# Kernel optimization log

Hardware: AMD Instinct MI355X
Metric: run time of the kernel (lower is better)

## Reference

```python
import jax, jax.numpy as jnp
import numpy as np

HEAD_DIM = 256
N_HEADS = 8
ROPE_BASE = 10000.0
EPS = 1e-6


def _rms(x):
    xf = x.astype(jnp.float32)
    return xf * jax.lax.rsqrt(jnp.mean(xf * xf, axis=-1, keepdims=True) + EPS)


def _rotate_half(x):
    x1, x2 = jnp.split(x, 2, axis=-1)
    return jnp.concatenate([-x2, x1], axis=-1)


def _mlp(h, wg, wu, wd):
    # Gemma gated MLP with gelu_pytorch_tanh activation
    return (jax.nn.gelu(h @ wg, approximate=True) * (h @ wu)) @ wd


def _qkv(h, wq, wk, wv):
    B, S, _ = h.shape
    q = (h @ wq).reshape(B, S, N_HEADS, HEAD_DIM).transpose(0, 2, 1, 3)  # [B,H,S,Dh]
    k = (h @ wk).reshape(B, S, HEAD_DIM)                                  # MQA: 1 kv head
    v = (h @ wv).reshape(B, S, HEAD_DIM)
    return q, k, v


def _forward(x_prefix, x_expert, attention_mask, adarms_cond, position_ids,
             p_ln1, p_wq, p_wk, p_wv, p_wo, p_ln2, p_wgate, p_wup, p_wdown,
             e_ada1_w, e_ada1_b, e_wq, e_wk, e_wv, e_wo, e_ada2_w, e_ada2_b,
             e_wgate, e_wup, e_wdown):
    B, S1, Dp = x_prefix.shape
    S2 = x_expert.shape[1]

    # --- pre-attention norms: plain Gemma RMSNorm (prefix), AdaRMS (expert) ---
    h_p = _rms(x_prefix) * (1.0 + p_ln1)
    mod1 = adarms_cond @ e_ada1_w + e_ada1_b                  # [B, 3*De]
    sc1, sh1, g1 = jnp.split(mod1, 3, axis=-1)
    h_e = _rms(x_expert) * (1.0 + sc1[:, None]) + sh1[:, None]
    gate1_e = g1[:, None]                                      # [B,1,De]

    # --- concatenated QKV across the two streams ---
    q_p, k_p, v_p = _qkv(h_p, p_wq, p_wk, p_wv)
    q_e, k_e, v_e = _qkv(h_e, e_wq, e_wk, e_wv)
    q = jnp.concatenate([q_p, q_e], axis=2)                    # [B,H,S,Dh]
    k = jnp.concatenate([k_p, k_e], axis=1)                    # [B,S,Dh]
    v = jnp.concatenate([v_p, v_e], axis=1)

    # --- rotary embedding on joint positions ---
    inv_freq = 1.0 / (ROPE_BASE ** (jnp.arange(0, HEAD_DIM, 2, dtype=jnp.float32) / HEAD_DIM))
    ang = position_ids.astype(jnp.float32)[..., None] * inv_freq
    emb = jnp.concatenate([ang, ang], axis=-1)                 # [B,S,Dh]
    cos, sin = jnp.cos(emb), jnp.sin(emb)
    q = q * cos[:, None] + _rotate_half(q) * sin[:, None]
    k = k * cos + _rotate_half(k) * sin

    # --- eager MQA attention ---
    scaling = HEAD_DIM ** -0.5
    scores = jnp.einsum('bhqd,bkd->bhqk', q, k) * scaling + attention_mask
    probs = jax.nn.softmax(scores.astype(jnp.float32), axis=-1)
    att = jnp.einsum('bhqk,bkd->bhqd', probs, v)
    att = att.transpose(0, 2, 1, 3).reshape(B, S1 + S2, N_HEADS * HEAD_DIM)

    # --- prefix stream: o_proj, residual, RMSNorm, gated MLP, residual ---
    res_p = x_prefix + att[:, :S1] @ p_wo
    h2_p = _rms(res_p) * (1.0 + p_ln2)
    out_p = res_p + _mlp(h2_p, p_wgate, p_wup, p_wdown)

    # --- expert stream: gated residuals from AdaRMS ---
    res_e = x_expert + gate1_e * (att[:, S1:] @ e_wo)
    mod2 = adarms_cond @ e_ada2_w + e_ada2_b
    sc2, sh2, g2 = jnp.split(mod2, 3, axis=-1)
    h2_e = _rms(res_e) * (1.0 + sc2[:, None]) + sh2[:, None]
    out_e = res_e + g2[:, None] * _mlp(h2_e, e_wgate, e_wup, e_wdown)
    return out_p, out_e


def setup_inputs() -> dict:
    key = jax.random.key(0)
    ks = iter(jax.random.split(key, 32))
    B, S1, S2 = 4, 768, 64
    Dp, De, Dh, H = 2048, 1024, 256, 8
    Fp, Fe = 16384, 4096

    def w(shape, s=0.02):
        return jax.random.normal(next(ks), shape, dtype=jnp.float32) * s

    return dict(
        x_prefix=jax.random.normal(next(ks), (B, S1, Dp), dtype=jnp.float32),
        x_expert=jax.random.normal(next(ks), (B, S2, De), dtype=jnp.float32),
        attention_mask=jnp.zeros((B, 1, S1 + S2, S1 + S2), dtype=jnp.float32),
        adarms_cond=jax.random.normal(next(ks), (B, De), dtype=jnp.float32),
        position_ids=jnp.sort(jax.random.randint(next(ks), (B, S1 + S2), 0, S1 + S2), axis=-1),
        p_ln1=jnp.zeros((Dp,), jnp.float32),
        p_wq=w((Dp, H * Dh)), p_wk=w((Dp, Dh)), p_wv=w((Dp, Dh)), p_wo=w((H * Dh, Dp)),
        p_ln2=jnp.zeros((Dp,), jnp.float32),
        p_wgate=w((Dp, Fp)), p_wup=w((Dp, Fp)), p_wdown=w((Fp, Dp)),
        e_ada1_w=w((De, 3 * De)), e_ada1_b=jnp.zeros((3 * De,), jnp.float32),
        e_wq=w((De, H * Dh)), e_wk=w((De, Dh)), e_wv=w((De, Dh)), e_wo=w((H * Dh, De)),
        e_ada2_w=w((De, 3 * De)), e_ada2_b=jnp.zeros((3 * De,), jnp.float32),
        e_wgate=w((De, Fe)), e_wup=w((De, Fe)), e_wdown=w((Fe, De)),
    )


def reference(x_prefix, x_expert, attention_mask, adarms_cond, position_ids,
              p_ln1, p_wq, p_wk, p_wv, p_wo, p_ln2, p_wgate, p_wup, p_wdown,
              e_ada1_w, e_ada1_b, e_wq, e_wk, e_wv, e_wo, e_ada2_w, e_ada2_b,
              e_wgate, e_wup, e_wdown):
    return _forward(x_prefix, x_expert, attention_mask, adarms_cond, position_ids,
                    p_ln1, p_wq, p_wk, p_wv, p_wo, p_ln2, p_wgate, p_wup, p_wdown,
                    e_ada1_w, e_ada1_b, e_wq, e_wk, e_wv, e_wo, e_ada2_w, e_ada2_b,
                    e_wgate, e_wup, e_wdown)
```

## Files before the change

kernel.cpp:

```cpp
#include <hip/hip_runtime.h>
#include <stdint.h>

typedef unsigned short ushort_t;
typedef __attribute__((ext_vector_type(8))) short short8;
typedef __attribute__((ext_vector_type(4))) float f32x4;

#define DEVINL __device__ __forceinline__

DEVINL ushort_t f2bf(float f){
  union { float f; uint32_t u; } v; v.f = f;
  uint32_t u = v.u;
  uint32_t r = (u + 0x7fffu + ((u >> 16) & 1u)) >> 16;
  return (ushort_t)r;
}
DEVINL float bf2f(ushort_t h){
  union { uint32_t u; float f; } v; v.u = ((uint32_t)h) << 16;
  return v.f;
}
DEVINL f32x4 mfma16(short8 a, short8 b, f32x4 c){
  return __builtin_amdgcn_mfma_f32_16x16x32_bf16(a, b, c, 0, 0, 0);
}
DEVINL void gload_lds16(const void* g, void* l){
  __builtin_amdgcn_global_load_lds((const __attribute__((address_space(1))) void*)g,
                                   (__attribute__((address_space(3))) void*)l, 16, 0, 0);
}
DEVINL float gelu_tanh(float x){
  return 0.5f * x * (1.f + tanhf(0.7978845608028654f * (x + 0.044715f * x * x * x)));
}

#define BAR() __builtin_amdgcn_s_barrier()
#define LGK0() asm volatile("s_waitcnt lgkmcnt(0)" ::: "memory")
#define VMC4() asm volatile("s_waitcnt vmcnt(4)" ::: "memory")
#define VMC0() asm volatile("s_waitcnt vmcnt(0)" ::: "memory")
#define PRIO1() __builtin_amdgcn_s_setprio(1)
#define PRIO0() __builtin_amdgcn_s_setprio(0)

__global__ void transpose_bf16(const float* __restrict__ W, ushort_t* __restrict__ Wt,
                               int K, int N)
{
  __shared__ ushort_t tile[64 * 65];
  const int t = threadIdx.x;
  const int k0 = blockIdx.y * 64, n0 = blockIdx.x * 64;
#pragma unroll
  for (int rr = 0; rr < 4; ++rr){
    const int row = rr * 16 + (t >> 4);
    const int c4 = (t & 15) * 4;
    float4 v = *(const float4*)&W[(size_t)(k0 + row) * N + n0 + c4];
    ushort_t* dst = &tile[row * 65 + c4];
    dst[0] = f2bf(v.x); dst[1] = f2bf(v.y); dst[2] = f2bf(v.z); dst[3] = f2bf(v.w);
  }
  __syncthreads();
  const int n = t >> 2, kc = (t & 3) * 16;
  __align__(16) ushort_t tmp[16];
#pragma unroll
  for (int j = 0; j < 16; ++j) tmp[j] = tile[(kc + j) * 65 + n];
  ushort_t* out = &Wt[(size_t)(n0 + n) * K + k0 + kc];
  *(short8*)&out[0] = *(short8*)&tmp[0];
  *(short8*)&out[8] = *(short8*)&tmp[8];
}

__global__ void mod_kernel(const float* __restrict__ cond,
                           const float* __restrict__ w1, const float* __restrict__ b1,
                           const float* __restrict__ w2, const float* __restrict__ b2,
                           float* __restrict__ mod1, float* __restrict__ mod2)
{
  __shared__ float cs[1024];
  const int bid = blockIdx.x, tid = threadIdx.x;
  const int which = bid / 48, rem = bid % 48, b = rem / 12, j0 = (rem % 12) * 256;
  const float* W = which ? w2 : w1;
  const float* bias = which ? b2 : b1;
  float* out = which ? mod2 : mod1;
#pragma unroll
  for (int i = 0; i < 4; ++i) cs[i * 256 + tid] = cond[b * 1024 + i * 256 + tid];
  __syncthreads();
  const int j = j0 + tid;
  float acc = bias[j];
  for (int k = 0; k < 1024; ++k) acc = fmaf(cs[k], W[(size_t)k * 3072 + j], acc);
  out[b * 3072 + j] = acc;
}

__global__ void rms_kernel(const float* __restrict__ x, ushort_t* __restrict__ out, int D,
                           const float* __restrict__ sw, const float* __restrict__ sh,
                           int mod_rpb, int mod_stride)
{
  const int row = blockIdx.x, tid = threadIdx.x;
  const float* xr = x + (size_t)row * D;
  const int nc = D >> 10;
  float ss = 0.f;
  for (int c = 0; c < nc; ++c){
    float4 v = *(const float4*)&xr[c * 1024 + tid * 4];
    ss += v.x * v.x + v.y * v.y + v.z * v.z + v.w * v.w;
  }
  for (int o = 32; o > 0; o >>= 1) ss += __shfl_xor(ss, o);
  __shared__ float red[4];
  if ((tid & 63) == 0) red[tid >> 6] = ss;
  __syncthreads();
  const float scale = rsqrtf((red[0] + red[1] + red[2] + red[3]) / (float)D + 1e-6f);
  const float* swp = sw;
  const float* shp = sh;
  if (mod_rpb){
    int bb = row / mod_rpb;
    swp += (size_t)bb * mod_stride;
    if (shp) shp += (size_t)bb * mod_stride;
  }
  for (int c = 0; c < nc; ++c){
    const int d = c * 1024 + tid * 4;
    float4 v = *(const float4*)&xr[d];
    float vv[4] = {v.x, v.y, v.z, v.w};
#pragma unroll
    for (int i = 0; i < 4; ++i){
      float tv = vv[i] * scale * (1.f + swp[d + i]);
      if (shp) tv += shp[d + i];
      out[(size_t)row * D + d + i] = f2bf(tv);
    }
  }
}

__global__ void rope_kernel(const ushort_t* __restrict__ qkv_p, const ushort_t* __restrict__ qkv_e,
                            const int* __restrict__ pos_ids,
                            ushort_t* __restrict__ q_all, ushort_t* __restrict__ k_all,
                            ushort_t* __restrict__ vT)
{
  const int tok = blockIdx.x, tid = threadIdx.x;
  int b, s;
  const ushort_t* src;
  if (tok < 3072){ b = tok / 768; s = tok - b * 768; src = qkv_p + (size_t)tok * 2560; }
  else { int te = tok - 3072; b = te >> 6; s = 768 + (te & 63); src = qkv_e + (size_t)te * 2560; }
  const int pos = pos_ids[b * 832 + s];
  __shared__ float cs[128], sn[128];
  if (tid < 128){
    float f = powf(10000.f, -(float)tid * (1.f / 128.f));
    float a = (float)pos * f;
    cs[tid] = cosf(a); sn[tid] = sinf(a);
  }
  __syncthreads();
#pragma unroll
  for (int c = 0; c < 10; ++c){
    const int n = c * 256 + tid;
    const float v = bf2f(src[n]);
    if (n < 2048){
      const int h = n >> 8, d = n & 255;
      const float o = bf2f(src[(h << 8) + ((d < 128) ? (d + 128) : (d - 128))]);
      const int dd = d & 127;
      const float r = (d < 128) ? v * cs[dd] - o * sn[dd] : v * cs[dd] + o * sn[dd];
      q_all[(((size_t)(b * 8 + h)) * 832 + s) * 256 + d] = f2bf(r);
    } else if (n < 2304){
      const int d = n - 2048;
      const float o = bf2f(src[2048 + ((d < 128) ? (d + 128) : (d - 128))]);
      const int dd = d & 127;
      const float r = (d < 128) ? v * cs[dd] - o * sn[dd] : v * cs[dd] + o * sn[dd];
      k_all[((size_t)(b * 832) + s) * 256 + d] = f2bf(r);
    } else {
      const int d = n - 2304;
      vT[((size_t)(b * 256) + d) * 832 + s] = src[n];
    }
  }
}

__global__ void __launch_bounds__(256, 2)
attn_kernel(const ushort_t* __restrict__ q_all, const ushort_t* __restrict__ k_all,
            const ushort_t* __restrict__ vT, const float* __restrict__ mask,
            ushort_t* __restrict__ att)
{
  __shared__ __align__(16) ushort_t Ks[64 * 256];
  __shared__ __align__(16) ushort_t Vs[256 * 64];
  __shared__ __align__(16) ushort_t Ps[4][16 * 72];
  const int tid = threadIdx.x, lane = tid & 63, wid = tid >> 6;
  const int l15 = lane & 15, lg = lane >> 4;
  const int qt = blockIdx.x, h = blockIdx.y, b = blockIdx.z;
  const int q0 = qt * 64 + wid * 16;

  short8 qf[8];
  {
    const ushort_t* qr = q_all + (((size_t)(b * 8 + h) * 832) + q0 + l15) * 256;
#pragma unroll
    for (int s = 0; s < 8; ++s) qf[s] = *(const short8*)&qr[s * 32 + lg * 8];
  }

  f32x4 accO[16] = {};
  float mrow[4] = {-3.0e38f, -3.0e38f, -3.0e38f, -3.0e38f};
  float lrow[4] = {0.f, 0.f, 0.f, 0.f};

  for (int kt = 0; kt < 13; ++kt){
    const int s0 = kt * 64;
#pragma unroll
    for (int i = 0; i < 8; ++i){
      const int o = i * 256 + tid;
      gload_lds16(k_all + ((size_t)(b * 832) + s0 + (o >> 5)) * 256 + (o & 31) * 8, &Ks[o * 8]);
      gload_lds16(vT + ((size_t)(b * 256) + (o >> 3)) * 832 + s0 + (o & 7) * 8, &Vs[o * 8]);
    }
    __syncthreads();

    f32x4 sc[4] = {};
#pragma unroll
    for (int s = 0; s < 8; ++s){
#pragma unroll
      for (int nf = 0; nf < 4; ++nf){
        short8 kb = *(const short8*)&Ks[(nf * 16 + l15) * 256 + s * 32 + lg * 8];
        sc[nf] = mfma16(qf[s], kb, sc[nf]);
      }
    }
#pragma unroll
    for (int nf = 0; nf < 4; ++nf){
#pragma unroll
      for (int r = 0; r < 4; ++r){
        const int q = q0 + lg * 4 + r;
        const int kk = s0 + nf * 16 + l15;
        sc[nf][r] = sc[nf][r] * 0.0625f + mask[((size_t)b * 832 + q) * 832 + kk];
      }
    }
    float al[4];
#pragma unroll
    for (int r = 0; r < 4; ++r){
      float tm = fmaxf(fmaxf(sc[0][r], sc[1][r]), fmaxf(sc[2][r], sc[3][r]));
      tm = fmaxf(tm, __shfl_xor(tm, 1));
      tm = fmaxf(tm, __shfl_xor(tm, 2));
      tm = fmaxf(tm, __shfl_xor(tm, 4));
      tm = fmaxf(tm, __shfl_xor(tm, 8));
      const float mnew = fmaxf(mrow[r], tm);
      al[r] = __expf(mrow[r] - mnew);
      mrow[r] = mnew;
      float rs = 0.f;
#pragma unroll
      for (int nf = 0; nf < 4; ++nf){
        const float p = __expf(sc[nf][r] - mnew);
        rs += p;
        Ps[wid][(lg * 4 + r) * 72 + nf * 16 + l15] = f2bf(p);
      }
      rs += __shfl_xor(rs, 1);
      rs += __shfl_xor(rs, 2);
      rs += __shfl_xor(rs, 4);
      rs += __shfl_xor(rs, 8);
      lrow[r] = lrow[r] * al[r] + rs;
    }
#pragma unroll
    for (int nd = 0; nd < 16; ++nd){
#pragma unroll
      for (int r = 0; r < 4; ++r) accO[nd][r] *= al[r];
    }
#pragma unroll
    for (int ks = 0; ks < 2; ++ks){
      short8 pa = *(const short8*)&Ps[wid][l15 * 72 + ks * 32 + lg * 8];
#pragma unroll
      for (int nd = 0; nd < 16; ++nd){
        short8 vb = *(const short8*)&Vs[(nd * 16 + l15) * 64 + ks * 32 + lg * 8];
        accO[nd] = mfma16(pa, vb, accO[nd]);
      }
    }
    __syncthreads();
  }
#pragma unroll
  for (int nd = 0; nd < 16; ++nd){
#pragma unroll
    for (int r = 0; r < 4; ++r){
      const int q = q0 + lg * 4 + r;
      const int d = nd * 16 + l15;
      att[((size_t)(b * 832) + q) * 2048 + h * 256 + d] = f2bf(accO[nd][r] / lrow[r]);
    }
  }
}

template<int EPI>
__global__ void __launch_bounds__(256, 2)
gemm_bt(const ushort_t* __restrict__ A, int lda, int a_rpb, int a_bstride, int a_r0,
        const ushort_t* __restrict__ Bt, int ldb,
        void* __restrict__ Cv, int N, int K,
        const void* __restrict__ Xv,
        const float* __restrict__ gatep, int gate_stride, int gate_rpb,
        size_t pstride)
{
  __shared__ __align__(16) ushort_t As[128 * 64];
  __shared__ __align__(16) ushort_t Bs[128 * 64];
  const int tid = threadIdx.x;
  const int lane = tid & 63;
  const int l15 = lane & 15, lg = lane >> 4;
  const int wid = tid >> 6;
  const int wm = (wid >> 1) * 64, wn = (wid & 1) * 64;
  const int m0 = blockIdx.y * 128, n0 = blockIdx.x * 128;
  const int z = blockIdx.z;
  const int kbeg = z * K, kend = z * K + K;

  size_t abase[4], bbase[4];
  const int k8 = (tid & 7) * 8;
#pragma unroll
  for (int i = 0; i < 4; ++i){
    const int row = (i * 256 + tid) >> 3;
    const int r = m0 + row;
    const int bb = r / a_rpb;
    const int arow = bb * a_bstride + a_r0 + (r - bb * a_rpb);
    abase[i] = (size_t)arow * lda + k8;
    bbase[i] = (size_t)(n0 + row) * ldb + k8;
  }

  f32x4 acc[4][4] = {};

  for (int kt = kbeg; kt < kend; kt += 64){
#pragma unroll
    for (int i = 0; i < 4; ++i){
      gload_lds16(A + abase[i] + kt, &As[(i * 256 + tid) * 8]);
      gload_lds16(Bt + bbase[i] + kt, &Bs[(i * 256 + tid) * 8]);
    }
    __syncthreads();
#pragma unroll
    for (int s = 0; s < 2; ++s){
      const int ko = s * 32 + lg * 8;
      short8 af[4], bfr[4];
#pragma unroll
      for (int i = 0; i < 4; ++i) af[i] = *(const short8*)&As[(wm + i * 16 + l15) * 64 + ko];
#pragma unroll
      for (int j = 0; j < 4; ++j) bfr[j] = *(const short8*)&Bs[(wn + j * 16 + l15) * 64 + ko];
#pragma unroll
      for (int i = 0; i < 4; ++i)
#pragma unroll
        for (int j = 0; j < 4; ++j)
          acc[i][j] = mfma16(af[i], bfr[j], acc[i][j]);
    }
    __syncthreads();
  }

#pragma unroll
  for (int i = 0; i < 4; ++i){
#pragma unroll
    for (int r = 0; r < 4; ++r){
      const int m = m0 + wm + i * 16 + lg * 4 + r;
#pragma unroll
      for (int j = 0; j < 4; ++j){
        const int n = n0 + wn + j * 16 + l15;
        const size_t idx = (size_t)m * N + n;
        const float v = acc[i][j][r];
        if (EPI == 0){
          ((ushort_t*)Cv)[idx] = f2bf(v);
        } else if (EPI == 1){
          const float g = bf2f(((const ushort_t*)Xv)[idx]);
          ((ushort_t*)Cv)[idx] = f2bf(gelu_tanh(g) * v);
        } else if (EPI == 2){
          ((float*)Cv)[idx] = ((const float*)Xv)[idx] + v;
        } else if (EPI == 3){
          const int bb = m / gate_rpb;
          ((float*)Cv)[idx] = ((const float*)Xv)[idx] + gatep[(size_t)bb * gate_stride + n] * v;
        } else {
          ((float*)Cv)[(size_t)z * pstride + idx] = v;
        }
      }
    }
  }
}

#define MMAQ(AF, BF, MQ, NQ) \
  { _Pragma("unroll") for (int i_ = 0; i_ < 4; ++i_){ \
      _Pragma("unroll") for (int j_ = 0; j_ < 2; ++j_){ \
        _Pragma("unroll") for (int s_ = 0; s_ < 2; ++s_){ \
          acc[(MQ)*4 + i_][(NQ)*2 + j_] = \
            mfma16(AF[i_][s_], BF[j_][s_], acc[(MQ)*4 + i_][(NQ)*2 + j_]); } } } }

#define READA(F, BUF, OA) \
  { _Pragma("unroll") for (int i_ = 0; i_ < 4; ++i_){ \
      _Pragma("unroll") for (int s_ = 0; s_ < 2; ++s_){ \
        F[i_][s_] = *(const short8*)&(BUF)[OA[i_][s_]]; } } }

#define READB(F, BUF, OB) \
  { _Pragma("unroll") for (int j_ = 0; j_ < 2; ++j_){ \
      _Pragma("unroll") for (int s_ = 0; s_ < 2; ++s_){ \
        F[j_][s_] = *(const short8*)&(BUF)[OB[j_][s_]]; } } }

template<int EPI>
__global__ void __launch_bounds__(512, 1)
gemm8(const ushort_t* __restrict__ A, int lda,
      const ushort_t* __restrict__ Bt, int ldb,
      void* __restrict__ Cv, int N, int klen,
      const void* __restrict__ Xv, size_t pstride)
{
  __shared__ __align__(16) ushort_t As[2][256 * 64];
  __shared__ __align__(16) ushort_t Bs[2][256 * 64];

  const int tid = threadIdx.x;
  const int lane = tid & 63, wid = tid >> 6;
  const int l15 = lane & 15, lg = lane >> 4;
  const int wm = (wid >> 2) * 128, wn = (wid & 3) * 64;

  const int gx = gridDim.x, gy = gridDim.y, nwg = gx * gy;
  const int orig = blockIdx.y * gx + blockIdx.x;
  const int q = nwg >> 3, r = nwg & 7;
  const int xcd = orig & 7, lo = orig >> 3;
  const int wg = (xcd < r ? xcd * (q + 1) : r * (q + 1) + (xcd - r) * q) + lo;
  const int m0 = (wg % gy) * 256, n0 = (wg / gy) * 256;
  const int z = blockIdx.z;
  const size_t k0 = (size_t)z * klen;
  const int NT = klen >> 6;

  uint32_t offA0[4][2], offA1[4][2], offB0[2][2], offB1[2][2];
#pragma unroll
  for (int i = 0; i < 4; ++i){
#pragma unroll
    for (int s = 0; s < 2; ++s){
      int r0 = wm + 0 * 64 + i * 16 + l15;
      int r1 = wm + 1 * 64 + i * 16 + l15;
      offA0[i][s] = r0 * 64 + (((s * 4 + lg) ^ (r0 & 7)) << 3);
      offA1[i][s] = r1 * 64 + (((s * 4 + lg) ^ (r1 & 7)) << 3);
    }
  }
#pragma unroll
  for (int j = 0; j < 2; ++j){
#pragma unroll
    for (int s = 0; s < 2; ++s){
      int r0 = wn + 0 * 32 + j * 16 + l15;
      int r1 = wn + 1 * 32 + j * 16 + l15;
      offB0[j][s] = r0 * 64 + (((s * 4 + lg) ^ (r0 & 7)) << 3);
      offB1[j][s] = r1 * 64 + (((s * 4 + lg) ^ (r1 & 7)) << 3);
    }
  }

  const ushort_t* gptr[4][2];
  uint32_t ldso[2];
#pragma unroll
  for (int c = 0; c < 2; ++c){
    const int idx = c * 512 + tid;
    const int row = idx >> 3, slot = idx & 7;
    const uint32_t sw = (uint32_t)((slot ^ (row & 7)) << 3);
    ldso[c] = (uint32_t)idx * 8;
    gptr[0][c] = A  + (size_t)(m0 + row) * lda + k0 + sw;
    gptr[1][c] = A  + (size_t)(m0 + 128 + row) * lda + k0 + sw;
    gptr[2][c] = Bt + (size_t)(n0 + row) * ldb + k0 + sw;
    gptr[3][c] = Bt + (size_t)(n0 + 128 + row) * ldb + k0 + sw;
  }

  auto stage = [&](int buf, int half, int kt){
    ushort_t* base = (half < 2) ? &As[buf][(half & 1) * 8192] : &Bs[buf][(half & 1) * 8192];
#pragma unroll
    for (int c = 0; c < 2; ++c)
      gload_lds16(gptr[half][c] + kt, base + ldso[c]);
  };

  stage(0, 0, 0); stage(0, 1, 0); stage(0, 2, 0); stage(0, 3, 0);
  if (NT > 1){ stage(1, 2, 64); stage(1, 3, 64); VMC4(); } else { VMC0(); }
  BAR();

  short8 af[4][2], bq0[2][2], bq1[2][2];
  f32x4 acc[8][4] = {};

  for (int t = 0; t < NT; ++t){
    const int cur = t & 1, nxt = cur ^ 1;
    const int kc1 = (t + 1) << 6, kc2 = (t + 2) << 6;
    const ushort_t* Ac = As[cur];
    const ushort_t* Bc = Bs[cur];
    READA(af, Ac, offA0);
    READB(bq0, Bc, offB0);
    READB(bq1, Bc, offB1);
    if (t + 1 < NT){ stage(nxt, 0, kc1); stage(nxt, 1, kc1); }
    BAR(); LGK0();
    PRIO1(); MMAQ(af, bq0, 0, 0); MMAQ(af, bq1, 0, 1); PRIO0(); BAR();
    READA(af, Ac, offA1);
    if (t + 2 < NT){ stage(cur, 2, kc2); stage(cur, 3, kc2); VMC4(); } else { VMC0(); }
    BAR(); LGK0();
    PRIO1(); MMAQ(af, bq1, 1, 1); MMAQ(af, bq0, 1, 0); PRIO0(); BAR();
  }

#pragma unroll
  for (int i = 0; i < 8; ++i){
#pragma unroll
    for (int rr = 0; rr < 4; ++rr){
      const int m = m0 + wm + i * 16 + lg * 4 + rr;
#pragma unroll
      for (int j = 0; j < 4; ++j){
        const int n = n0 + wn + j * 16 + l15;
        const size_t idx = (size_t)m * N + n;
        const float v = acc[i][j][rr];
        if (EPI == 0){
          ((ushort_t*)Cv)[idx] = f2bf(v);
        } else if (EPI == 1){
          const float g = bf2f(((const ushort_t*)Xv)[idx]);
          ((ushort_t*)Cv)[idx] = f2bf(gelu_tanh(g) * v);
        } else {
          ((float*)Cv)[(size_t)z * pstride + idx] = v;
        }
      }
    }
  }
}

__global__ void reduce4(const float* __restrict__ part, const float* __restrict__ res,
                        float* __restrict__ out, int total4, size_t pstride)
{
  int i = blockIdx.x * blockDim.x + threadIdx.x;
  const int stride = gridDim.x * blockDim.x;
  for (; i < total4; i += stride){
    const size_t e = (size_t)i * 4;
    float4 a = *(const float4*)&res[e];
#pragma unroll
    for (int z = 0; z < 4; ++z){
      float4 p = *(const float4*)&part[(size_t)z * pstride + e];
      a.x += p.x; a.y += p.y; a.z += p.z; a.w += p.w;
    }
    *(float4*)&out[e] = a;
  }
}

__global__ void fuse_gelu(const float* __restrict__ pg, const float* __restrict__ pu,
                          ushort_t* __restrict__ out, int total4, size_t pstride)
{
  int i = blockIdx.x * blockDim.x + threadIdx.x;
  const int stride = gridDim.x * blockDim.x;
  for (; i < total4; i += stride){
    const size_t e = (size_t)i * 4;
    float4 g = *(const float4*)&pg[e];
    float4 u = *(const float4*)&pu[e];
#pragma unroll
    for (int z = 1; z < 4; ++z){
      float4 a = *(const float4*)&pg[(size_t)z * pstride + e];
      float4 b = *(const float4*)&pu[(size_t)z * pstride + e];
      g.x += a.x; g.y += a.y; g.z += a.z; g.w += a.w;
      u.x += b.x; u.y += b.y; u.z += b.z; u.w += b.w;
    }
    out[e + 0] = f2bf(gelu_tanh(g.x) * u.x);
    out[e + 1] = f2bf(gelu_tanh(g.y) * u.y);
    out[e + 2] = f2bf(gelu_tanh(g.z) * u.z);
    out[e + 3] = f2bf(gelu_tanh(g.w) * u.w);
  }
}

__global__ void reduce_gated(const float* __restrict__ part, size_t pstride, int nz,
                             const float* __restrict__ base, const float* __restrict__ gate,
                             int gstride, int rpb, int N,
                             float* __restrict__ out, int total4)
{
  int i = blockIdx.x * blockDim.x + threadIdx.x;
  const int stride = gridDim.x * blockDim.x;
  for (; i < total4; i += stride){
    const size_t e = (size_t)i * 4;
    const int row = (int)(e / N), n = (int)(e % N);
    const int b = row / rpb;
    float4 s = *(const float4*)&part[e];
    for (int z = 1; z < nz; ++z){
      float4 p = *(const float4*)&part[(size_t)z * pstride + e];
      s.x += p.x; s.y += p.y; s.z += p.z; s.w += p.w;
    }
    float4 bs = *(const float4*)&base[e];
    const float* gp = &gate[(size_t)b * gstride + n];
    bs.x += gp[0] * s.x; bs.y += gp[1] * s.y; bs.z += gp[2] * s.z; bs.w += gp[3] * s.w;
    *(float4*)&out[e] = bs;
  }
}

extern "C" void kernel_launch(void* const* d_in, const int* in_sizes, int n_in,
                              void* d_out, int out_size, void* d_ws, size_t ws_size,
                              hipStream_t stream)
{
  const float* x_prefix = (const float*)d_in[0];
  const float* x_expert = (const float*)d_in[1];
  const float* mask     = (const float*)d_in[2];
  const float* cond     = (const float*)d_in[3];
  const int*   pos      = (const int*)d_in[4];
  const float* p_ln1    = (const float*)d_in[5];
  const float* p_wq     = (const float*)d_in[6];
  const float* p_wk     = (const float*)d_in[7];
  const float* p_wv     = (const float*)d_in[8];
  const float* p_wo     = (const float*)d_in[9];
  const float* p_ln2    = (const float*)d_in[10];
  const float* p_wgate  = (const float*)d_in[11];
  const float* p_wup    = (const float*)d_in[12];
  const float* p_wdown  = (const float*)d_in[13];
  const float* e_ada1_w = (const float*)d_in[14];
  const float* e_ada1_b = (const float*)d_in[15];
  const float* e_wq     = (const float*)d_in[16];
  const float* e_wk     = (const float*)d_in[17];
  const float* e_wv     = (const float*)d_in[18];
  const float* e_wo     = (const float*)d_in[19];
  const float* e_ada2_w = (const float*)d_in[20];
  const float* e_ada2_b = (const float*)d_in[21];
  const float* e_wgate  = (const float*)d_in[22];
  const float* e_wup    = (const float*)d_in[23];
  const float* e_wdown  = (const float*)d_in[24];

  char* ws = (char*)d_ws;
  size_t off = 0;
  auto alloc = [&](size_t bytes) -> char* {
    char* p = ws + off;
    off += bytes;
    off = (off + 255) & ~(size_t)255;
    return p;
  };

  ushort_t* t_wqkv_p  = (ushort_t*)alloc((size_t)2560 * 2048 * 2);
  ushort_t* t_wo_p    = (ushort_t*)alloc((size_t)2048 * 2048 * 2);
  ushort_t* t_wgate_p = (ushort_t*)alloc((size_t)16384 * 2048 * 2);
  ushort_t* t_wup_p   = (ushort_t*)alloc((size_t)16384 * 2048 * 2);
  ushort_t* t_wdown_p = (ushort_t*)alloc((size_t)2048 * 16384 * 2);
  ushort_t* t_wqkv_e  = (ushort_t*)alloc((size_t)2560 * 1024 * 2);
  ushort_t* t_wo_e    = (ushort_t*)alloc((size_t)1024 * 2048 * 2);
  ushort_t* t_wgate_e = (ushort_t*)alloc((size_t)4096 * 1024 * 2);
  ushort_t* t_wup_e   = (ushort_t*)alloc((size_t)4096 * 1024 * 2);
  ushort_t* t_wdown_e = (ushort_t*)alloc((size_t)1024 * 4096 * 2);
  float* mod1 = (float*)alloc((size_t)4 * 3072 * 4);
  float* mod2 = (float*)alloc((size_t)4 * 3072 * 4);
  float* res_p = (float*)alloc((size_t)3072 * 2048 * 4);
  float* res_e = (float*)alloc((size_t)256 * 1024 * 4);
  ushort_t* h2_p = (ushort_t*)alloc((size_t)3072 * 2048 * 2);
  ushort_t* h2_e = (ushort_t*)alloc((size_t)256 * 1024 * 2);
  ushort_t* g_e  = (ushort_t*)alloc((size_t)256 * 4096 * 2);

  const size_t zone_off = off;
  ushort_t* h_p   = (ushort_t*)alloc((size_t)3072 * 2048 * 2);
  ushort_t* h_e   = (ushort_t*)alloc((size_t)256 * 1024 * 2);
  ushort_t* qkv_p = (ushort_t*)alloc((size_t)3072 * 2560 * 2);
  ushort_t* qkv_e = (ushort_t*)alloc((size_t)256 * 2560 * 2);
  ushort_t* q_all = (ushort_t*)alloc((size_t)4 * 8 * 832 * 256 * 2);
  ushort_t* k_all = (ushort_t*)alloc((size_t)4 * 832 * 256 * 2);
  ushort_t* vTb   = (ushort_t*)alloc((size_t)4 * 256 * 832 * 2);
  ushort_t* att   = (ushort_t*)alloc((size_t)4 * 832 * 2048 * 2);
  const size_t phase1_end = off;
  ushort_t* g_p = (ushort_t*)(ws + zone_off);

  float* partials = (float*)t_wgate_p;
  const size_t PSTRIDE_P = (size_t)3072 * 2048;
  float* pwo = (float*)(ws + zone_off);
  const size_t PSTRIDE_E = (size_t)256 * 1024;
  float* pg = (float*)t_wgate_p;
  float* pu = pg + (size_t)4 * 256 * 4096;
  float* pd = pu + (size_t)4 * 256 * 4096;
  const size_t PSTRIDE_GE = (size_t)256 * 4096;

  const size_t g_p_end = zone_off + (size_t)3072 * 16384 * 2;
  const size_t needed = (phase1_end > g_p_end) ? phase1_end : g_p_end;
  if (ws_size < needed) return;

  const int BIG = 1 << 30;

  transpose_bf16<<<dim3(2048/64, 2048/64), 256, 0, stream>>>(p_wq, t_wqkv_p, 2048, 2048);
  transpose_bf16<<<dim3(256/64, 2048/64), 256, 0, stream>>>(p_wk, t_wqkv_p + (size_t)2048*2048, 2048, 256);
  transpose_bf16<<<dim3(256/64, 2048/64), 256, 0, stream>>>(p_wv, t_wqkv_p + (size_t)2304*2048, 2048, 256);
  transpose_bf16<<<dim3(2048/64, 2048/64), 256, 0, stream>>>(p_wo, t_wo_p, 2048, 2048);
  transpose_bf16<<<dim3(16384/64, 2048/64), 256, 0, stream>>>(p_wgate, t_wgate_p, 2048, 16384);
  transpose_bf16<<<dim3(16384/64, 2048/64), 256, 0, stream>>>(p_wup, t_wup_p, 2048, 16384);
  transpose_bf16<<<dim3(2048/64, 16384/64), 256, 0, stream>>>(p_wdown, t_wdown_p, 16384, 2048);
  transpose_bf16<<<dim3(2048/64, 1024/64), 256, 0, stream>>>(e_wq, t_wqkv_e, 1024, 2048);
  transpose_bf16<<<dim3(256/64, 1024/64), 256, 0, stream>>>(e_wk, t_wqkv_e + (size_t)2048*1024, 1024, 256);
  transpose_bf16<<<dim3(256/64, 1024/64), 256, 0, stream>>>(e_wv, t_wqkv_e + (size_t)2304*1024, 1024, 256);
  transpose_bf16<<<dim3(1024/64, 2048/64), 256, 0, stream>>>(e_wo, t_wo_e, 2048, 1024);
  transpose_bf16<<<dim3(4096/64, 1024/64), 256, 0, stream>>>(e_wgate, t_wgate_e, 1024, 4096);
  transpose_bf16<<<dim3(4096/64, 1024/64), 256, 0, stream>>>(e_wup, t_wup_e, 1024, 4096);
  transpose_bf16<<<dim3(1024/64, 4096/64), 256, 0, stream>>>(e_wdown, t_wdown_e, 4096, 1024);

  mod_kernel<<<96, 256, 0, stream>>>(cond, e_ada1_w, e_ada1_b, e_ada2_w, e_ada2_b, mod1, mod2);

  rms_kernel<<<3072, 256, 0, stream>>>(x_prefix, h_p, 2048, p_ln1, nullptr, 0, 0);
  rms_kernel<<<256, 256, 0, stream>>>(x_expert, h_e, 1024, mod1, mod1 + 1024, 64, 3072);

  gemm_bt<0><<<dim3(20, 24), 256, 0, stream>>>(h_p, 2048, BIG, 0, 0, t_wqkv_p, 2048,
                                               qkv_p, 2560, 2048, nullptr, nullptr, 0, 1, 0);
  gemm_bt<0><<<dim3(20, 2), 256, 0, stream>>>(h_e, 1024, BIG, 0, 0, t_wqkv_e, 1024,
                                              qkv_e, 2560, 1024, nullptr, nullptr, 0, 1, 0);

  rope_kernel<<<3328, 256, 0, stream>>>(qkv_p, qkv_e, pos, q_all, k_all, vTb);

  attn_kernel<<<dim3(13, 8, 4), 256, 0, stream>>>(q_all, k_all, vTb, mask, att);

  gemm_bt<2><<<dim3(16, 24), 256, 0, stream>>>(att, 2048, 768, 832, 0, t_wo_p, 2048,
                                               res_p, 2048, 2048, x_prefix, nullptr, 0, 1, 0);
  gemm_bt<4><<<dim3(8, 2, 4), 256, 0, stream>>>(att, 2048, 64, 832, 768, t_wo_e, 2048,
                                                pwo, 1024, 512, nullptr, nullptr, 0, 1, PSTRIDE_E);
  reduce_gated<<<256, 256, 0, stream>>>(pwo, PSTRIDE_E, 4, x_expert, mod1 + 2048, 3072, 64, 1024,
                                        res_e, (256 * 1024) / 4);

  rms_kernel<<<3072, 256, 0, stream>>>(res_p, h2_p, 2048, p_ln2, nullptr, 0, 0);
  rms_kernel<<<256, 256, 0, stream>>>(res_e, h2_e, 1024, mod2, mod2 + 1024, 64, 3072);

  gemm8<0><<<dim3(64, 12, 1), 512, 0, stream>>>(h2_p, 2048, t_wgate_p, 2048,
                                                g_p, 16384, 2048, nullptr, 0);
  gemm8<1><<<dim3(64, 12, 1), 512, 0, stream>>>(h2_p, 2048, t_wup_p, 2048,
                                                g_p, 16384, 2048, g_p, 0);
  gemm8<4><<<dim3(8, 12, 4), 512, 0, stream>>>(g_p, 16384, t_wdown_p, 16384,
                                               partials, 2048, 4096, nullptr, PSTRIDE_P);
  reduce4<<<2048, 256, 0, stream>>>(partials, res_p, (float*)d_out,
                                    (3072 * 2048) / 4, PSTRIDE_P);

  gemm_bt<4><<<dim3(32, 2, 4), 256, 0, stream>>>(h2_e, 1024, BIG, 0, 0, t_wgate_e, 1024,
                                                 pg, 4096, 256, nullptr, nullptr, 0, 1, PSTRIDE_GE);
  gemm_bt<4><<<dim3(32, 2, 4), 256, 0, stream>>>(h2_e, 1024, BIG, 0, 0, t_wup_e, 1024,
                                                 pu, 4096, 256, nullptr, nullptr, 0, 1, PSTRIDE_GE);
  fuse_gelu<<<1024, 256, 0, stream>>>(pg, pu, g_e, (256 * 4096) / 4, PSTRIDE_GE);
  gemm_bt<4><<<dim3(8, 2, 8), 256, 0, stream>>>(g_e, 4096, BIG, 0, 0, t_wdown_e, 4096,
                                                pd, 1024, 512, nullptr, nullptr, 0, 1, PSTRIDE_E);
  reduce_gated<<<256, 256, 0, stream>>>(pd, PSTRIDE_E, 8, res_e, mod2 + 2048, 3072, 64, 1024,
                                        (float*)d_out + (size_t)3072 * 2048, (256 * 1024) / 4);
}
```

Before: 1.293 ms.

## Restructure GEMM main loop into eight-phase ping-pong with finer-grained staged loads

The double-buffered GEMM mainloop is unrolled by two and split into eight MFMA quadrant phases. Each phase issues one quarter-tile global-to-LDS load, in the style of the HipKittens 8-wave schedule, with a vmcnt(6) wait so more loads stay in flight. The goal is to overlap memory traffic with MFMA work more evenly and shorten the stalls between compute blocks. It adds more barriers and assumes NT is even and at least 2, since the prologue now stages the second buffer unconditionally.

```diff
diff --git a/kernel.cpp b/kernel.cpp
--- a/kernel.cpp
+++ b/kernel.cpp
@@ -30,6 +30,7 @@
 
 #define BAR() __builtin_amdgcn_s_barrier()
 #define LGK0() asm volatile("s_waitcnt lgkmcnt(0)" ::: "memory")
+#define VMC6() asm volatile("s_waitcnt vmcnt(6)" ::: "memory")
 #define VMC4() asm volatile("s_waitcnt vmcnt(4)" ::: "memory")
 #define VMC0() asm volatile("s_waitcnt vmcnt(0)" ::: "memory")
 #define PRIO1() __builtin_amdgcn_s_setprio(1)
@@ -431,28 +432,48 @@
       gload_lds16(gptr[half][c] + kt, base + ldso[c]);
   };
 
-  stage(0, 0, 0); stage(0, 1, 0); stage(0, 2, 0); stage(0, 3, 0);
-  if (NT > 1){ stage(1, 2, 64); stage(1, 3, 64); VMC4(); } else { VMC0(); }
-  BAR();
+  stage(0, 2, 0); stage(0, 3, 0); stage(0, 0, 0); stage(0, 1, 0);
+  stage(1, 2, 64); stage(1, 3, 64); stage(1, 0, 64);
+  VMC6(); BAR();
 
   short8 af[4][2], bq0[2][2], bq1[2][2];
   f32x4 acc[8][4] = {};
 
-  for (int t = 0; t < NT; ++t){
-    const int cur = t & 1, nxt = cur ^ 1;
-    const int kc1 = (t + 1) << 6, kc2 = (t + 2) << 6;
-    const ushort_t* Ac = As[cur];
-    const ushort_t* Bc = Bs[cur];
-    READA(af, Ac, offA0);
-    READB(bq0, Bc, offB0);
-    READB(bq1, Bc, offB1);
-    if (t + 1 < NT){ stage(nxt, 0, kc1); stage(nxt, 1, kc1); }
+  for (int t = 0; t < NT; t += 2){
+    const int kc1 = (t + 1) << 6, kc2 = (t + 2) << 6, kc3 = (t + 3) << 6;
+    const bool more = (t + 2 < NT);
+    READA(af, As[0], offA0);
+    READB(bq0, Bs[0], offB0);
+    stage(1, 1, kc1);
     BAR(); LGK0();
-    PRIO1(); MMAQ(af, bq0, 0, 0); MMAQ(af, bq1, 0, 1); PRIO0(); BAR();
-    READA(af, Ac, offA1);
-    if (t + 2 < NT){ stage(cur, 2, kc2); stage(cur, 3, kc2); VMC4(); } else { VMC0(); }
+    PRIO1(); MMAQ(af, bq0, 0, 0); PRIO0(); BAR();
+    READB(bq1, Bs[0], offB1);
+    if (more) stage(0, 2, kc2);
     BAR(); LGK0();
-    PRIO1(); MMAQ(af, bq1, 1, 1); MMAQ(af, bq0, 1, 0); PRIO0(); BAR();
+    PRIO1(); MMAQ(af, bq1, 0, 1); PRIO0(); BAR();
+    READA(af, As[0], offA1);
+    if (more) stage(0, 3, kc2);
+    BAR(); LGK0();
+    PRIO1(); MMAQ(af, bq1, 1, 1); PRIO0(); BAR();
+    if (more){ stage(0, 0, kc2); VMC6(); } else { VMC0(); }
+    BAR();
+    PRIO1(); MMAQ(af, bq0, 1, 0); PRIO0(); BAR();
+    READA(af, As[1], offA0);
+    READB(bq0, Bs[1], offB0);
+    if (more) stage(0, 1, kc2);
+    BAR(); LGK0();
+    PRIO1(); MMAQ(af, bq0, 0, 0); PRIO0(); BAR();
+    READB(bq1, Bs[1], offB1);
+    if (more) stage(1, 2, kc3);
+    BAR(); LGK0();
+    PRIO1(); MMAQ(af, bq1, 0, 1); PRIO0(); BAR();
+    READA(af, As[1], offA1);
+    if (more) stage(1, 3, kc3);
+    BAR(); LGK0();
+    PRIO1(); MMAQ(af, bq1, 1, 1); PRIO0(); BAR();
+    if (more){ stage(1, 0, kc3); VMC6(); } else { VMC0(); }
+    BAR();
+    PRIO1(); MMAQ(af, bq0, 1, 0); PRIO0(); BAR();
   }
 
 #pragma unroll
```

Result: slower. 1.350 ms (+4.3%).

## Fuse prefix gate and up projections into one dual-accumulator GEMM kernel

Applied to the files above, without the earlier changes.

Replaces the two separate gate and up GEMMs for the prefix MLP, which wrote the gate output to memory and reread it for the GELU product, with one kernel that loads the shared activation tile once and accumulates both projections, applying GELU-tanh times up in the epilogue. This saves a full bf16 intermediate write and read and one reload of the activations. The new kernel is simple: single-buffered LDS with no overlap of loads and compute, 128x128 tiles, and doubled accumulator registers. Compared with the tuned 512-thread gemm8 it may lose pipelining efficiency and occupancy.

```diff
diff --git a/kernel.cpp b/kernel.cpp
--- a/kernel.cpp
+++ b/kernel.cpp
@@ -341,6 +341,77 @@
         } else {
           ((float*)Cv)[(size_t)z * pstride + idx] = v;
         }
+      }
+    }
+  }
+}
+
+__global__ void __launch_bounds__(256)
+gemm_gu(const ushort_t* __restrict__ A, int lda,
+        const ushort_t* __restrict__ Bg, const ushort_t* __restrict__ Bu, int ldb,
+        ushort_t* __restrict__ G, int N, int K)
+{
+  __shared__ __align__(16) ushort_t As[128 * 64];
+  __shared__ __align__(16) ushort_t Bgs[128 * 64];
+  __shared__ __align__(16) ushort_t Bus[128 * 64];
+  const int tid = threadIdx.x;
+  const int lane = tid & 63;
+  const int l15 = lane & 15, lg = lane >> 4;
+  const int wid = tid >> 6;
+  const int wm = (wid >> 1) * 64, wn = (wid & 1) * 64;
+  const int m0 = blockIdx.y * 128, n0 = blockIdx.x * 128;
+
+  size_t abase[4], bbase[4];
+  const int k8 = (tid & 7) * 8;
+#pragma unroll
+  for (int i = 0; i < 4; ++i){
+    const int row = (i * 256 + tid) >> 3;
+    abase[i] = (size_t)(m0 + row) * lda + k8;
+    bbase[i] = (size_t)(n0 + row) * ldb + k8;
+  }
+
+  f32x4 accG[4][4] = {};
+  f32x4 accU[4][4] = {};
+
+  for (int kt = 0; kt < K; kt += 64){
+#pragma unroll
+    for (int i = 0; i < 4; ++i){
+      gload_lds16(A  + abase[i] + kt, &As [(i * 256 + tid) * 8]);
+      gload_lds16(Bg + bbase[i] + kt, &Bgs[(i * 256 + tid) * 8]);
+      gload_lds16(Bu + bbase[i] + kt, &Bus[(i * 256 + tid) * 8]);
+    }
+    __syncthreads();
+#pragma unroll
+    for (int s = 0; s < 2; ++s){
+      const int ko = s * 32 + lg * 8;
+      short8 af[4], bg[4], bu[4];
+#pragma unroll
+      for (int i = 0; i < 4; ++i) af[i] = *(const short8*)&As [(wm + i * 16 + l15) * 64 + ko];
+#pragma unroll
+      for (int j = 0; j < 4; ++j) bg[j] = *(const short8*)&Bgs[(wn + j * 16 + l15) * 64 + ko];
+#pragma unroll
+      for (int j = 0; j < 4; ++j) bu[j] = *(const short8*)&Bus[(wn + j * 16 + l15) * 64 + ko];
+#pragma unroll
+      for (int i = 0; i < 4; ++i){
+#pragma unroll
+        for (int j = 0; j < 4; ++j){
+          accG[i][j] = mfma16(af[i], bg[j], accG[i][j]);
+          accU[i][j] = mfma16(af[i], bu[j], accU[i][j]);
+        }
+      }
+    }
+    __syncthreads();
+  }
+
+#pragma unroll
+  for (int i = 0; i < 4; ++i){
+#pragma unroll
+    for (int r = 0; r < 4; ++r){
+      const int m = m0 + wm + i * 16 + lg * 4 + r;
+#pragma unroll
+      for (int j = 0; j < 4; ++j){
+        const int n = n0 + wn + j * 16 + l15;
+        G[(size_t)m * N + n] = f2bf(gelu_tanh(accG[i][j][r]) * accU[i][j][r]);
       }
     }
   }
@@ -664,10 +735,8 @@
   rms_kernel<<<3072, 256, 0, stream>>>(res_p, h2_p, 2048, p_ln2, nullptr, 0, 0);
   rms_kernel<<<256, 256, 0, stream>>>(res_e, h2_e, 1024, mod2, mod2 + 1024, 64, 3072);
 
-  gemm8<0><<<dim3(64, 12, 1), 512, 0, stream>>>(h2_p, 2048, t_wgate_p, 2048,
-                                                g_p, 16384, 2048, nullptr, 0);
-  gemm8<1><<<dim3(64, 12, 1), 512, 0, stream>>>(h2_p, 2048, t_wup_p, 2048,
-                                                g_p, 16384, 2048, g_p, 0);
+  gemm_gu<<<dim3(128, 24), 256, 0, stream>>>(h2_p, 2048, t_wgate_p, t_wup_p, 2048,
+                                             g_p, 16384, 2048);
   gemm8<4><<<dim3(8, 12, 4), 512, 0, stream>>>(g_p, 16384, t_wdown_p, 16384,
                                                partials, 2048, 4096, nullptr, PSTRIDE_P);
   reduce4<<<2048, 256, 0, stream>>>(partials, res_p, (float*)d_out,
```

New measurement: 1.805 ms. +39.5%, slower.

## Swizzle K/V layouts for bank-conflict-free attention loads; remap GEMM blocks per XCD

Applied to the files above, without the earlier changes.

The RoPE/prep kernel now writes K and V^T with an XOR swizzle on 8-element chunks, and the attention kernel reads LDS with the matching XOR index. This removes LDS bank conflicts on the strided K and V fragment reads. Separately, the GEMM remaps the linear workgroup id so consecutive tiles land on the same XCD and walks M fastest, aiming for better L2 reuse of B tiles. The swizzle changes the stored layout of k_all/vT, so any other consumer of those buffers would need the same mapping.

```diff
diff --git a/kernel.cpp b/kernel.cpp
--- a/kernel.cpp
+++ b/kernel.cpp
@@ -149,10 +149,15 @@
       const float o = bf2f(src[2048 + ((d < 128) ? (d + 128) : (d - 128))]);
       const int dd = d & 127;
       const float r = (d < 128) ? v * cs[dd] - o * sn[dd] : v * cs[dd] + o * sn[dd];
-      k_all[((size_t)(b * 832) + s) * 256 + d] = f2bf(r);
+      const int ck = d >> 3, e = d & 7;
+      const int ck2 = ck ^ (s & 7);
+      k_all[((size_t)(b * 832) + s) * 256 + (ck2 << 3) + e] = f2bf(r);
     } else {
       const int d = n - 2304;
-      vT[((size_t)(b * 256) + d) * 832 + s] = src[n];
+      const int stile = s >> 6, sl = s & 63;
+      const int cv = sl >> 3, e = sl & 7;
+      const int cv2 = cv ^ (d & 7);
+      vT[((size_t)(b * 256) + d) * 832 + (stile << 6) + (cv2 << 3) + e] = src[n];
     }
   }
 }
@@ -169,6 +174,7 @@
   const int l15 = lane & 15, lg = lane >> 4;
   const int qt = blockIdx.x, h = blockIdx.y, b = blockIdx.z;
   const int q0 = qt * 64 + wid * 16;
+  const int x7 = l15 & 7;
 
   short8 qf[8];
   {
@@ -196,7 +202,7 @@
     for (int s = 0; s < 8; ++s){
 #pragma unroll
       for (int nf = 0; nf < 4; ++nf){
-        short8 kb = *(const short8*)&Ks[(nf * 16 + l15) * 256 + s * 32 + lg * 8];
+        short8 kb = *(const short8*)&Ks[(nf * 16 + l15) * 256 + (((s * 4 + lg) ^ x7) << 3)];
         sc[nf] = mfma16(qf[s], kb, sc[nf]);
       }
     }
@@ -243,7 +249,7 @@
       short8 pa = *(const short8*)&Ps[wid][l15 * 72 + ks * 32 + lg * 8];
 #pragma unroll
       for (int nd = 0; nd < 16; ++nd){
-        short8 vb = *(const short8*)&Vs[(nd * 16 + l15) * 64 + ks * 32 + lg * 8];
+        short8 vb = *(const short8*)&Vs[(nd * 16 + l15) * 64 + (((ks * 4 + lg) ^ x7) << 3)];
         accO[nd] = mfma16(pa, vb, accO[nd]);
       }
     }
@@ -276,7 +282,12 @@
   const int l15 = lane & 15, lg = lane >> 4;
   const int wid = tid >> 6;
   const int wm = (wid >> 1) * 64, wn = (wid & 1) * 64;
-  const int m0 = blockIdx.y * 128, n0 = blockIdx.x * 128;
+  const int gx = gridDim.x, gy = gridDim.y, nwg = gx * gy;
+  const int orig = blockIdx.y * gx + blockIdx.x;
+  const int q = nwg >> 3, r = nwg & 7;
+  const int xcd = orig & 7, lo = orig >> 3;
+  const int wg = (xcd < r ? xcd * (q + 1) : r * (q + 1) + (xcd - r) * q) + lo;
+  const int m0 = (wg % gy) * 128, n0 = (wg / gy) * 128;
   const int z = blockIdx.z;
   const int kbeg = z * K, kend = z * K + K;
 
@@ -285,9 +296,9 @@
 #pragma unroll
   for (int i = 0; i < 4; ++i){
     const int row = (i * 256 + tid) >> 3;
-    const int r = m0 + row;
-    const int bb = r / a_rpb;
-    const int arow = bb * a_bstride + a_r0 + (r - bb * a_rpb);
+    const int rr = m0 + row;
+    const int bb = rr / a_rpb;
+    const int arow = bb * a_bstride + a_r0 + (rr - bb * a_rpb);
     abase[i] = (size_t)arow * lda + k8;
     bbase[i] = (size_t)(n0 + row) * ldb + k8;
   }
@@ -321,13 +332,13 @@
 #pragma unroll
   for (int i = 0; i < 4; ++i){
 #pragma unroll
-    for (int r = 0; r < 4; ++r){
-      const int m = m0 + wm + i * 16 + lg * 4 + r;
+    for (int rr = 0; rr < 4; ++rr){
+      const int m = m0 + wm + i * 16 + lg * 4 + rr;
 #pragma unroll
       for (int j = 0; j < 4; ++j){
         const int n = n0 + wn + j * 16 + l15;
         const size_t idx = (size_t)m * N + n;
-        const float v = acc[i][j][r];
+        const float v = acc[i][j][rr];
         if (EPI == 0){
           ((ushort_t*)Cv)[idx] = f2bf(v);
         } else if (EPI == 1){
```

New measurement: 1.269 ms. No clear change (-1.9%).
